# Kernel optimization log

Measured on AMD Instinct MI355X. Metric: run time of the kernel, lower is better.

## Reference

```python
import jax, jax.numpy as jnp
import numpy as np
from jax.scipy.special import erf

B, S, D, H, F = 2, 2048, 1024, 16, 4096
EPS = 1e-5


def setup_inputs() -> dict:
    key = jax.random.key(0)
    ks = jax.random.split(key, 7)
    s = 0.02  # init scale so attention logits stay in a sane range
    return {
        "x": jax.random.normal(ks[0], (B, S, D), jnp.float32),
        "wq": jax.random.normal(ks[1], (D, D), jnp.float32) * s,
        "wk": jax.random.normal(ks[2], (D, D), jnp.float32) * s,
        "wv": jax.random.normal(ks[3], (D, D), jnp.float32) * s,
        "wo": jax.random.normal(ks[4], (D, D), jnp.float32) * s,
        "w1": jax.random.normal(ks[5], (F, D), jnp.float32) * s,
        "w2": jax.random.normal(ks[6], (D, F), jnp.float32) * s,
        "g1": jnp.ones((D,), jnp.float32),
        "g2": jnp.ones((D,), jnp.float32),
    }


def _rmsnorm(x, g):
    return x / jnp.sqrt(jnp.mean(x * x, axis=-1, keepdims=True) + EPS) * g


def _gelu_exact(x):
    # 0.5 * x * (1 + erf(x / sqrt(2)))
    return 0.5 * x * (1.0 + erf(x * (1.0 / np.sqrt(2.0).astype(np.float32))))


def reference(x, wq, wk, wv, wo, w1, w2, g1, g2):
    b, s, d = x.shape
    dk = d // H
    # --- attention sublayer (pre-RMSNorm) ---
    h = _rmsnorm(x, g1)
    # Linear(bias=False): y = h @ W.T; split heads -> [b, H, s, dk]
    q = (h @ wq.T).reshape(b, s, H, dk).transpose(0, 2, 1, 3)
    k = (h @ wk.T).reshape(b, s, H, dk).transpose(0, 2, 1, 3)
    v = (h @ wv.T).reshape(b, s, H, dk).transpose(0, 2, 1, 3)
    scores = jnp.einsum('bhqd,bhkd->bhqk', q, k) / jnp.sqrt(jnp.float32(dk))
    causal = jnp.triu(jnp.ones((s, s), bool), 1)  # True above diagonal -> masked
    scores = jnp.where(causal, -jnp.inf, scores)
    attn = jax.nn.softmax(scores, axis=-1)
    o = jnp.einsum('bhqk,bhkd->bhqd', attn, v)
    o = o.transpose(0, 2, 1, 3).reshape(b, s, d) @ wo.T
    x = x + o
    # --- FFN sublayer (pre-RMSNorm, exact-erf GELU) ---
    h2 = _rmsnorm(x, g2)
    f = _gelu_exact(h2 @ w1.T) @ w2.T
    return x + f
```

## Files before the change

### kernel.cpp

```cpp
#include <hip/hip_runtime.h>
#include <hip/hip_bf16.h>
#include <math.h>

#define B_   2
#define S_   2048
#define D_   1024
#define H_   16
#define DK_  64
#define F_   4096
#define NTOK (B_ * S_)

typedef __bf16 bf16x8 __attribute__((ext_vector_type(8)));
typedef float  f32x4  __attribute__((ext_vector_type(4)));

__device__ __forceinline__ unsigned short bf16r(float f) {
  unsigned u = __builtin_bit_cast(unsigned, f);
  u += 0x7fffu + ((u >> 16) & 1u);
  return (unsigned short)(u >> 16);
}

__device__ __forceinline__ void gload_lds16(const void* g, void* l) {
  __builtin_amdgcn_global_load_lds(
      (__attribute__((address_space(1))) void*)g,
      (__attribute__((address_space(3))) void*)l, 16, 0, 0);
}

__device__ __forceinline__ unsigned lds_off(void* p) {
  return (unsigned)(size_t)(__attribute__((address_space(3))) void*)p;
}
__device__ __forceinline__ bf16x8 ds_read16(unsigned a) {
  bf16x8 r;
  asm volatile("ds_read_b128 %0, %1" : "=v"(r) : "v"(a));
  return r;
}
__device__ __forceinline__ void ds_write32(unsigned a, unsigned v) {
  asm volatile("ds_write_b32 %0, %1" : : "v"(a), "v"(v));
}
__device__ __forceinline__ float fexp2(float x) {
  float r;
  asm volatile("v_exp_f32 %0, %1\n\ts_nop 0" : "=v"(r) : "v"(x));
  return r;
}
__device__ __forceinline__ unsigned cvt_pk_bf16(float lo, float hi) {
  unsigned r;
  asm volatile("v_cvt_pk_bf16_f32 %0, %1, %2" : "=v"(r) : "v"(lo), "v"(hi));
  return r;
}

__device__ __forceinline__ float gelu_fast(float x) {
  float y = 0.7978845608f * x * (1.0f + 0.044715f * x * x);
  float e = fexp2(2.885390082f * y);
  float t = 1.0f - 2.0f / (e + 1.0f);
  return 0.5f * x * (1.0f + t);
}

#define QSCL 0.18033688f

struct CvtArgs {
  const float* src[6];
  unsigned short* dst[6];
  int start[7];
};
__global__ __launch_bounds__(256) void cvt_all_kernel(CvtArgs a) {
  int i = blockIdx.x * blockDim.x + threadIdx.x;
  if (i >= a.start[6]) return;
  int k = 0;
#pragma unroll
  for (int j = 1; j < 6; ++j)
    if (i >= a.start[j]) k = j;
  int off = i - a.start[k];
  float4 v = reinterpret_cast<const float4*>(a.src[k])[off];
  ushort4 o;
  o.x = bf16r(v.x); o.y = bf16r(v.y); o.z = bf16r(v.z); o.w = bf16r(v.w);
  reinterpret_cast<ushort4*>(a.dst[k])[off] = o;
}

__global__ __launch_bounds__(256) void rmsnorm_kernel(
    const float* __restrict__ x, const float* __restrict__ g,
    unsigned short* __restrict__ out) {
  int row = blockIdx.x;
  int t = threadIdx.x, lane = t & 63, w = t >> 6;
  float4 v = reinterpret_cast<const float4*>(x + (size_t)row * D_)[t];
  float ss = v.x * v.x + v.y * v.y + v.z * v.z + v.w * v.w;
#pragma unroll
  for (int d = 1; d < 64; d <<= 1) ss += __shfl_xor(ss, d);
  __shared__ float red[4];
  if (lane == 0) red[w] = ss;
  __syncthreads();
  float tot = red[0] + red[1] + red[2] + red[3];
  float rstd = rsqrtf(tot * (1.0f / D_) + 1e-5f);
  float4 gv = reinterpret_cast<const float4*>(g)[t];
  ushort4 o;
  o.x = bf16r(v.x * rstd * gv.x);
  o.y = bf16r(v.y * rstd * gv.y);
  o.z = bf16r(v.z * rstd * gv.z);
  o.w = bf16r(v.w * rstd * gv.w);
  reinterpret_cast<ushort4*>(out + (size_t)row * D_)[t] = o;
}

template <int EPI>
__device__ __forceinline__ void gemm256_body(
    const unsigned short* __restrict__ A, const unsigned short* __restrict__ Bw,
    int M, int N, int K,
    unsigned short* __restrict__ outB, unsigned short* __restrict__ outB2,
    unsigned short* __restrict__ outB3) {
  constexpr int BUFU = 12288;
  __shared__ __attribute__((aligned(16))) unsigned short lds[3 * BUFU];
  const int t = threadIdx.x, lane = t & 63, w = t >> 6;
  const int wm = w >> 1, wn = w & 1;
  const int lg = lane >> 4, ln = lane & 15;

  const int gx = gridDim.x;
  int bid = blockIdx.y * gx + blockIdx.x;
  int xcd = bid & 7, c = bid >> 3;
  int RX = gx >> 2, RY = gridDim.y >> 1;
  int bx = (xcd & 3) * RX + (c % RX);
  int by = (xcd >> 2) * RY + (c / RX);
  const int m0 = by * 256, n0 = bx * 128;

  const int nt = K >> 5;

  auto stage = [&](int tile) {
    int buf = tile % 3;
    const int k0 = tile << 5;
    unsigned short* la = &lds[buf * BUFU];
    unsigned short* lb = la + 8192;
#pragma unroll
    for (int i = 0; i < 2; ++i) {
      int g = i * 512 + t;
      int Ln = g >> 3, p = g & 7, u = p ^ (Ln & 7);
      int row = 2 * Ln + (u >> 2), cg = u & 3;
      gload_lds16(A + (size_t)(m0 + row) * K + k0 + cg * 8, &la[g * 8]);
    }
    {
      int Ln = t >> 3, p = t & 7, u = p ^ (Ln & 7);
      int row = 2 * Ln + (u >> 2), cg = u & 3;
      gload_lds16(Bw + (size_t)(n0 + row) * K + k0 + cg * 8, &lb[t * 8]);
    }
  };

  stage(0);
  stage(1);

  const unsigned base0 = lds_off(lds);
  unsigned offA[4], offB[4];
#pragma unroll
  for (int m = 0; m < 4; ++m) {
    int r = wm * 64 + m * 16 + ln;
    int Ln = r >> 1, p = ((r & 1) * 4 + lg) ^ (Ln & 7);
    offA[m] = (unsigned)((Ln * 64 + p * 8) * 2);
  }
#pragma unroll
  for (int n = 0; n < 4; ++n) {
    int r = wn * 64 + n * 16 + ln;
    int Ln = r >> 1, p = ((r & 1) * 4 + lg) ^ (Ln & 7);
    offB[n] = (unsigned)(16384 + (Ln * 64 + p * 8) * 2);
  }

  f32x4 acc[4][4] = {};

  for (int tile = 0; tile < nt; ++tile) {
    if (tile + 1 < nt) { asm volatile("s_waitcnt vmcnt(3)"); }
    else               { asm volatile("s_waitcnt vmcnt(0)"); }
    __builtin_amdgcn_sched_barrier(0);
    __builtin_amdgcn_s_barrier();
    const unsigned bb = base0 + (unsigned)((tile % 3) * (BUFU * 2));
    bf16x8 af[4], bf0, bf1;
#pragma unroll
    for (int m = 0; m < 4; ++m) af[m] = ds_read16(bb + offA[m]);
    bf0 = ds_read16(bb + offB[0]);
    bf1 = ds_read16(bb + offB[1]);
    if (tile + 2 < nt) stage(tile + 2);
    asm volatile("s_waitcnt lgkmcnt(0)");
    __builtin_amdgcn_sched_barrier(0);
    __builtin_amdgcn_s_setprio(1);
#pragma unroll
    for (int m = 0; m < 4; ++m) {
      acc[m][0] = __builtin_amdgcn_mfma_f32_16x16x32_bf16(af[m], bf0, acc[m][0], 0, 0, 0);
      acc[m][1] = __builtin_amdgcn_mfma_f32_16x16x32_bf16(af[m], bf1, acc[m][1], 0, 0, 0);
    }
    __builtin_amdgcn_s_setprio(0);
    bf0 = ds_read16(bb + offB[2]);
    bf1 = ds_read16(bb + offB[3]);
    asm volatile("s_waitcnt lgkmcnt(0)");
    __builtin_amdgcn_sched_barrier(0);
    __builtin_amdgcn_s_setprio(1);
#pragma unroll
    for (int m = 0; m < 4; ++m) {
      acc[m][2] = __builtin_amdgcn_mfma_f32_16x16x32_bf16(af[m], bf0, acc[m][2], 0, 0, 0);
      acc[m][3] = __builtin_amdgcn_mfma_f32_16x16x32_bf16(af[m], bf1, acc[m][3], 0, 0, 0);
    }
    __builtin_amdgcn_s_setprio(0);
  }

  const int rbase = m0 + wm * 64 + lg * 4;
  const int cbase = n0 + wn * 64 + ln;
#pragma unroll
  for (int m = 0; m < 4; ++m) {
#pragma unroll
    for (int n = 0; n < 4; ++n) {
      int col = cbase + n * 16;
#pragma unroll
      for (int j = 0; j < 4; ++j) {
        int row = rbase + m * 16 + j;
        float v = acc[m][n][j];
        if (EPI == 1) {
          outB[(size_t)row * N + col] = bf16r(gelu_fast(v));
        } else {
          if (col < D_) {
            outB[(size_t)row * D_ + col] = bf16r(v * QSCL);
          } else if (col < 2 * D_) {
            outB2[(size_t)row * D_ + (col - D_)] = bf16r(v);
          } else {
            int bb2 = row >> 11, s = row & (S_ - 1);
            outB3[((size_t)(bb2 * D_) + (col - 2 * D_)) * S_ + s] = bf16r(v);
          }
        }
      }
    }
  }
}

__global__ __launch_bounds__(512, 4) void qkv_gemm(
    const unsigned short* __restrict__ A, const unsigned short* __restrict__ Bw,
    int M, int N, int K, unsigned short* o1, unsigned short* o2, unsigned short* o3) {
  gemm256_body<4>(A, Bw, M, N, K, o1, o2, o3);
}
__global__ __launch_bounds__(512, 4) void ffn1_gemm(
    const unsigned short* __restrict__ A, const unsigned short* __restrict__ Bw,
    int M, int N, int K, unsigned short* o1) {
  gemm256_body<1>(A, Bw, M, N, K, o1, nullptr, nullptr);
}

__device__ __forceinline__ void gemm128_body(
    const unsigned short* __restrict__ A, const unsigned short* __restrict__ Bw,
    int M, int N, int K,
    const float* __restrict__ resid, float* __restrict__ outF) {
  constexpr int BUFU = 256 * 32;
  __shared__ __attribute__((aligned(16))) unsigned short lds[4 * BUFU];
  const int t = threadIdx.x, lane = t & 63, w = t >> 6;
  const int wm = w >> 2, wn = w & 3;
  const int lg = lane >> 4, ln = lane & 15;

  const int gx = gridDim.x;
  int bid = blockIdx.y * gx + blockIdx.x;
  int RX = gx >> 2, RY = gridDim.y >> 1;
  int xcd = bid & 7, c = bid >> 3;
  int bx = (xcd & 3) * RX + (c % RX);
  int by = (xcd >> 2) * RY + (c / RX);
  const int m0 = by * 128, n0 = bx * 128;

  const int nt = K >> 5;

  auto stage = [&](int tile) {
    const int buf = tile & 3;
    const int k0 = tile << 5;
    unsigned short* la = &lds[buf * BUFU];
    unsigned short* lb = la + 4096;
    int Ln = t >> 3, p = t & 7, u = p ^ (Ln & 7);
    int row = 2 * Ln + (u >> 2), cg = u & 3;
    gload_lds16(A + (size_t)(m0 + row) * K + k0 + cg * 8, &la[t * 8]);
    gload_lds16(Bw + (size_t)(n0 + row) * K + k0 + cg * 8, &lb[t * 8]);
  };

  stage(0);
  if (nt > 1) stage(1);
  if (nt > 2) stage(2);

  const unsigned base0 = lds_off(lds);
  unsigned offA[4], offB[2];
#pragma unroll
  for (int m = 0; m < 4; ++m) {
    int r = wm * 64 + m * 16 + ln;
    int Ln = r >> 1, p = ((r & 1) * 4 + lg) ^ (Ln & 7);
    offA[m] = (unsigned)((Ln * 64 + p * 8) * 2);
  }
#pragma unroll
  for (int n = 0; n < 2; ++n) {
    int r = wn * 32 + n * 16 + ln;
    int Ln = r >> 1, p = ((r & 1) * 4 + lg) ^ (Ln & 7);
    offB[n] = (unsigned)(8192 + (Ln * 64 + p * 8) * 2);
  }

  f32x4 acc[4][2] = {};

  for (int tile = 0; tile < nt; ++tile) {
    const int rem = nt - 1 - tile;
    if (rem >= 2)      { asm volatile("s_waitcnt vmcnt(4)"); }
    else if (rem == 1) { asm volatile("s_waitcnt vmcnt(2)"); }
    else               { asm volatile("s_waitcnt vmcnt(0)"); }
    __builtin_amdgcn_sched_barrier(0);
    __builtin_amdgcn_s_barrier();
    const unsigned bb = base0 + (unsigned)((tile & 3) * (BUFU * 2));
    bf16x8 af[4], bf[2];
#pragma unroll
    for (int m = 0; m < 4; ++m) af[m] = ds_read16(bb + offA[m]);
#pragma unroll
    for (int n = 0; n < 2; ++n) bf[n] = ds_read16(bb + offB[n]);
    if (tile + 3 < nt) stage(tile + 3);
    asm volatile("s_waitcnt lgkmcnt(0)");
    __builtin_amdgcn_sched_barrier(0);
    __builtin_amdgcn_s_setprio(1);
#pragma unroll
    for (int m = 0; m < 4; ++m)
#pragma unroll
      for (int n = 0; n < 2; ++n)
        acc[m][n] = __builtin_amdgcn_mfma_f32_16x16x32_bf16(af[m], bf[n], acc[m][n], 0, 0, 0);
    __builtin_amdgcn_s_setprio(0);
  }

  const int rbase = m0 + wm * 64 + lg * 4;
  const int cbase = n0 + wn * 32 + ln;
#pragma unroll
  for (int m = 0; m < 4; ++m) {
#pragma unroll
    for (int n = 0; n < 2; ++n) {
      int col = cbase + n * 16;
#pragma unroll
      for (int j = 0; j < 4; ++j) {
        int row = rbase + m * 16 + j;
        outF[(size_t)row * N + col] = acc[m][n][j] + resid[(size_t)row * N + col];
      }
    }
  }
}

__global__ __launch_bounds__(512, 4) void wo_gemm(
    const unsigned short* __restrict__ A, const unsigned short* __restrict__ Bw,
    int M, int N, int K, const float* __restrict__ resid, float* __restrict__ outF) {
  gemm128_body(A, Bw, M, N, K, resid, outF);
}
__global__ __launch_bounds__(512, 4) void ffn2_gemm(
    const unsigned short* __restrict__ A, const unsigned short* __restrict__ Bw,
    int M, int N, int K, const float* __restrict__ resid, float* __restrict__ outF) {
  gemm128_body(A, Bw, M, N, K, resid, outF);
}

__global__ __launch_bounds__(256, 4) void attn_kernel(
    const unsigned short* __restrict__ qg, const unsigned short* __restrict__ kg,
    const unsigned short* __restrict__ vt, unsigned short* __restrict__ og) {
  __shared__ __attribute__((aligned(16))) unsigned short Kl[2][4096];
  __shared__ __attribute__((aligned(16))) unsigned short Vl[2][4096];
  __shared__ __attribute__((aligned(16))) unsigned short Pl[4][1024];
  const int t = threadIdx.x, lane = t & 63, w = t >> 6;
  const int lg = lane >> 4, ln = lane & 15;

  int bid = blockIdx.x;
  int nl = (bid & 7) * 128 + (bid >> 3);
  int bh = nl >> 5, qxr = nl & 31;
  int b = bh >> 4, h = bh & 15;
  int q0 = (31 - qxr) * 64;
  int qw = q0 + w * 16;

  bf16x8 aq[2];
  {
    const unsigned short* qp =
        qg + (size_t)(b * S_ + qw + ln) * D_ + h * DK_ + lg * 8;
    aq[0] = *reinterpret_cast<const bf16x8*>(qp);
    aq[1] = *reinterpret_cast<const bf16x8*>(qp + 32);
  }
  asm volatile("" : : "v"(aq[0]), "v"(aq[1]));

  float mr = -1e30f, lr = 0.f;
  f32x4 oacc[4] = {};
  const int nt = (q0 >> 6) + 1;

  auto stage = [&](int kt) {
    const int buf = kt & 1;
    const int kv0 = kt * 64;
#pragma unroll
    for (int i = 0; i < 2; ++i) {
      int g = i * 256 + t;
      int row = g >> 3, cg = g & 7, sg = cg ^ (row & 7);
      gload_lds16(kg + (size_t)(b * S_ + kv0 + row) * D_ + h * DK_ + sg * 8, &Kl[buf][g * 8]);
      gload_lds16(vt + (size_t)(b * D_ + h * DK_ + row) * S_ + kv0 + sg * 8, &Vl[buf][g * 8]);
    }
  };
  stage(0);

  const unsigned kbase = lds_off(&Kl[0][0]);
  const unsigned vbase = lds_off(&Vl[0][0]);
  const unsigned pbase = lds_off(&Pl[w][0]);

  auto ctile = [&](int kt, bool dm) {
    const unsigned kb = kbase + (unsigned)((kt & 1) * 8192);
    const unsigned vb = vbase + (unsigned)((kt & 1) * 8192);
    f32x4 sc[4] = {};
    bf16x8 kf[4];
#pragma unroll
    for (int n = 0; n < 4; ++n) {
      int r = n * 16 + ln;
      int cg0 = lg ^ (r & 7);
      kf[n] = ds_read16(kb + (unsigned)((r * 64 + cg0 * 8) * 2));
    }
    if (!dm) stage(kt + 1);
    asm volatile("s_waitcnt lgkmcnt(0)");
    __builtin_amdgcn_sched_barrier(0);
#pragma unroll
    for (int n = 0; n < 4; ++n)
      sc[n] = __builtin_amdgcn_mfma_f32_16x16x32_bf16(kf[n], aq[0], sc[n], 0, 0, 0);
#pragma unroll
    for (int n = 0; n < 4; ++n) {
      int r = n * 16 + ln;
      int cg1 = (4 + lg) ^ (r & 7);
      kf[n] = ds_read16(kb + (unsigned)((r * 64 + cg1 * 8) * 2));
    }
    asm volatile("s_waitcnt lgkmcnt(0)");
    __builtin_amdgcn_sched_barrier(0);
#pragma unroll
    for (int n = 0; n < 4; ++n)
      sc[n] = __builtin_amdgcn_mfma_f32_16x16x32_bf16(kf[n], aq[1], sc[n], 0, 0, 0);
    if (dm) {
      const int kv0 = kt * 64;
      const int qi = qw + ln;
#pragma unroll
      for (int n = 0; n < 4; ++n)
#pragma unroll
        for (int j = 0; j < 4; ++j)
          if ((kv0 + n * 16 + lg * 4 + j) > qi) sc[n][j] = -1e30f;
    }
    float t0 = fmaxf(sc[0][0], sc[0][1]), t1 = fmaxf(sc[0][2], sc[0][3]);
    float t2 = fmaxf(sc[1][0], sc[1][1]), t3 = fmaxf(sc[1][2], sc[1][3]);
    float t4 = fmaxf(sc[2][0], sc[2][1]), t5 = fmaxf(sc[2][2], sc[2][3]);
    float t6 = fmaxf(sc[3][0], sc[3][1]), t7 = fmaxf(sc[3][2], sc[3][3]);
    t0 = fmaxf(t0, t1); t2 = fmaxf(t2, t3); t4 = fmaxf(t4, t5); t6 = fmaxf(t6, t7);
    float mx = fmaxf(fmaxf(t0, t2), fmaxf(t4, t6));
    mx = fmaxf(mx, __shfl_xor(mx, 16));
    mx = fmaxf(mx, __shfl_xor(mx, 32));
    float mn = fmaxf(mr, mx);
    float ps = 0.f;
#pragma unroll
    for (int n = 0; n < 4; ++n)
#pragma unroll
      for (int j = 0; j < 4; ++j) {
        float p = fexp2(sc[n][j] - mn);
        sc[n][j] = p;
        ps += p;
      }
    if (__all(mx <= mr)) {
      lr += ps;
    } else {
      float sf = fexp2(mr - mn);
      mr = mn;
      lr = lr * sf + ps;
#pragma unroll
      for (int j = 0; j < 4; ++j) {
        float sfj = __shfl(sf, lg * 4 + j);
#pragma unroll
        for (int f = 0; f < 4; ++f) oacc[f][j] *= sfj;
      }
    }
#pragma unroll
    for (int n = 0; n < 4; ++n) {
      int kvc = n * 16 + lg * 4;
      int cg = (kvc >> 3) ^ (ln & 7);
      unsigned pa_addr = pbase + (unsigned)((ln * 64 + cg * 8 + (kvc & 7)) * 2);
      ds_write32(pa_addr, cvt_pk_bf16(sc[n][0], sc[n][1]));
      ds_write32(pa_addr + 4, cvt_pk_bf16(sc[n][2], sc[n][3]));
    }
    asm volatile("s_waitcnt lgkmcnt(0)");
    __builtin_amdgcn_sched_barrier(0);
#pragma unroll
    for (int c = 0; c < 2; ++c) {
      unsigned cgp = (unsigned)((c * 4 + lg) ^ (ln & 7));
      bf16x8 pa = ds_read16(pbase + (unsigned)(ln * 128) + cgp * 16);
      bf16x8 vf[4];
#pragma unroll
      for (int f = 0; f < 4; ++f) {
        int dv = f * 16 + ln;
        int cgv = (c * 4 + lg) ^ (dv & 7);
        vf[f] = ds_read16(vb + (unsigned)((dv * 64 + cgv * 8) * 2));
      }
      asm volatile("s_waitcnt lgkmcnt(0)");
      __builtin_amdgcn_sched_barrier(0);
#pragma unroll
      for (int f = 0; f < 4; ++f)
        oacc[f] = __builtin_amdgcn_mfma_f32_16x16x32_bf16(pa, vf[f], oacc[f], 0, 0, 0);
    }
  };

  for (int kt = 0; kt < nt - 1; ++kt) {
    asm volatile("s_waitcnt vmcnt(0)");
    __builtin_amdgcn_sched_barrier(0);
    __builtin_amdgcn_s_barrier();
    ctile(kt, false);
  }
  asm volatile("s_waitcnt vmcnt(0)");
  __builtin_amdgcn_sched_barrier(0);
  __builtin_amdgcn_s_barrier();
  ctile(nt - 1, true);

  lr += __shfl_xor(lr, 16);
  lr += __shfl_xor(lr, 32);
#pragma unroll
  for (int j = 0; j < 4; ++j) {
    float lj = __shfl(lr, lg * 4 + j);
    float inv = 1.0f / lj;
    int row = b * S_ + qw + lg * 4 + j;
#pragma unroll
    for (int f = 0; f < 4; ++f)
      og[(size_t)row * D_ + h * DK_ + f * 16 + ln] = bf16r(oacc[f][j] * inv);
  }
}

extern "C" void kernel_launch(void* const* d_in, const int* in_sizes, int n_in,
                              void* d_out, int out_size, void* d_ws, size_t ws_size,
                              hipStream_t stream) {
  const float* x  = (const float*)d_in[0];
  const float* wq = (const float*)d_in[1];
  const float* wk = (const float*)d_in[2];
  const float* wv = (const float*)d_in[3];
  const float* wo = (const float*)d_in[4];
  const float* w1 = (const float*)d_in[5];
  const float* w2 = (const float*)d_in[6];
  const float* g1 = (const float*)d_in[7];
  const float* g2 = (const float*)d_in[8];
  float* out = (float*)d_out;

  char* ws = (char*)d_ws;
  const size_t MB = 1024 * 1024;
  unsigned short* wqkv_b = (unsigned short*)(ws + 0 * MB);
  unsigned short* wo_b   = (unsigned short*)(ws + 6 * MB);
  unsigned short* w1_b   = (unsigned short*)(ws + 8 * MB);
  unsigned short* w2_b   = (unsigned short*)(ws + 16 * MB);
  unsigned short* h_b    = (unsigned short*)(ws + 24 * MB);
  unsigned short* q_b    = (unsigned short*)(ws + 32 * MB);
  unsigned short* k_b    = (unsigned short*)(ws + 40 * MB);
  unsigned short* vt_b   = (unsigned short*)(ws + 48 * MB);
  unsigned short* o_b    = (unsigned short*)(ws + 56 * MB);
  float*          x1     = (float*)(ws + 64 * MB);
  unsigned short* mid    = (unsigned short*)(ws + 80 * MB);

  CvtArgs ca;
  ca.src[0] = wq; ca.dst[0] = wqkv_b;
  ca.src[1] = wk; ca.dst[1] = wqkv_b + (size_t)D_ * D_;
  ca.src[2] = wv; ca.dst[2] = wqkv_b + (size_t)2 * D_ * D_;
  ca.src[3] = wo; ca.dst[3] = wo_b;
  ca.src[4] = w1; ca.dst[4] = w1_b;
  ca.src[5] = w2; ca.dst[5] = w2_b;
  int q4 = D_ * D_ / 4, f4 = F_ * D_ / 4;
  ca.start[0] = 0;
  ca.start[1] = q4;
  ca.start[2] = 2 * q4;
  ca.start[3] = 3 * q4;
  ca.start[4] = 4 * q4;
  ca.start[5] = 4 * q4 + f4;
  ca.start[6] = 4 * q4 + 2 * f4;
  cvt_all_kernel<<<(ca.start[6] + 255) / 256, 256, 0, stream>>>(ca);

  rmsnorm_kernel<<<NTOK, 256, 0, stream>>>(x, g1, h_b);

  qkv_gemm<<<dim3(3 * D_ / 128, NTOK / 256), dim3(512), 0, stream>>>(
      h_b, wqkv_b, NTOK, 3 * D_, D_, q_b, k_b, vt_b);

  attn_kernel<<<dim3(1024), dim3(256), 0, stream>>>(q_b, k_b, vt_b, o_b);

  wo_gemm<<<dim3(D_ / 128, NTOK / 128), dim3(512), 0, stream>>>(
      o_b, wo_b, NTOK, D_, D_, x, x1);

  rmsnorm_kernel<<<NTOK, 256, 0, stream>>>(x1, g2, h_b);

  ffn1_gemm<<<dim3(F_ / 128, NTOK / 256), dim3(512), 0, stream>>>(
      h_b, w1_b, NTOK, F_, D_, mid);

  ffn2_gemm<<<dim3(D_ / 128, NTOK / 128), dim3(512), 0, stream>>>(
      mid, w2_b, NTOK, D_, F_, x1, out);
}
```

Baseline: 248.8 us.

## Enlarge GEMM tiles to 256x256 and pair causal query tiles with 128-wide KV tiles

The shared QKV/FFN1 GEMM body now computes 256x256 output tiles instead of 256x128. Each warp handles 128 rows, and the A and B halves of the next stage are staged separately, interleaved with the two MFMA halves. The attention kernel now uses 128-key K/V tiles and has each block process two query tiles (31-pi and pi), so causal work is balanced across blocks while the grid is halved. This targets operand reuse and load imbalance, at the cost of a larger LDS footprint, lower occupancy (launch bounds drop to 2), and fewer blocks in the QKV GEMM (192) to spread over the CUs.

```diff
diff --git a/kernel.cpp b/kernel.cpp
--- a/kernel.cpp
+++ b/kernel.cpp
@@ -104,10 +104,10 @@
     int M, int N, int K,
     unsigned short* __restrict__ outB, unsigned short* __restrict__ outB2,
     unsigned short* __restrict__ outB3) {
-  constexpr int BUFU = 12288;
+  constexpr int BUFU = 16384;
   __shared__ __attribute__((aligned(16))) unsigned short lds[3 * BUFU];
   const int t = threadIdx.x, lane = t & 63, w = t >> 6;
-  const int wm = w >> 1, wn = w & 1;
+  const int wm = w >> 2, wn = w & 3;
   const int lg = lane >> 4, ln = lane & 15;
 
   const int gx = gridDim.x;
@@ -116,15 +116,13 @@
   int RX = gx >> 2, RY = gridDim.y >> 1;
   int bx = (xcd & 3) * RX + (c % RX);
   int by = (xcd >> 2) * RY + (c / RX);
-  const int m0 = by * 256, n0 = bx * 128;
+  const int m0 = by * 256, n0 = bx * 256;
 
   const int nt = K >> 5;
 
-  auto stage = [&](int tile) {
-    int buf = tile % 3;
+  auto stageA = [&](int tile) {
+    unsigned short* la = &lds[(tile % 3) * BUFU];
     const int k0 = tile << 5;
-    unsigned short* la = &lds[buf * BUFU];
-    unsigned short* lb = la + 8192;
 #pragma unroll
     for (int i = 0; i < 2; ++i) {
       int g = i * 512 + t;
@@ -132,21 +130,27 @@
       int row = 2 * Ln + (u >> 2), cg = u & 3;
       gload_lds16(A + (size_t)(m0 + row) * K + k0 + cg * 8, &la[g * 8]);
     }
-    {
-      int Ln = t >> 3, p = t & 7, u = p ^ (Ln & 7);
+  };
+  auto stageB = [&](int tile) {
+    unsigned short* lb = &lds[(tile % 3) * BUFU + 8192];
+    const int k0 = tile << 5;
+#pragma unroll
+    for (int i = 0; i < 2; ++i) {
+      int g = i * 512 + t;
+      int Ln = g >> 3, p = g & 7, u = p ^ (Ln & 7);
       int row = 2 * Ln + (u >> 2), cg = u & 3;
-      gload_lds16(Bw + (size_t)(n0 + row) * K + k0 + cg * 8, &lb[t * 8]);
+      gload_lds16(Bw + (size_t)(n0 + row) * K + k0 + cg * 8, &lb[g * 8]);
     }
   };
 
-  stage(0);
-  stage(1);
+  stageA(0); stageB(0);
+  stageA(1); stageB(1);
 
   const unsigned base0 = lds_off(lds);
-  unsigned offA[4], offB[4];
-#pragma unroll
-  for (int m = 0; m < 4; ++m) {
-    int r = wm * 64 + m * 16 + ln;
+  unsigned offA[8], offB[4];
+#pragma unroll
+  for (int m = 0; m < 8; ++m) {
+    int r = wm * 128 + m * 16 + ln;
     int Ln = r >> 1, p = ((r & 1) * 4 + lg) ^ (Ln & 7);
     offA[m] = (unsigned)((Ln * 64 + p * 8) * 2);
   }
@@ -157,46 +161,48 @@
     offB[n] = (unsigned)(16384 + (Ln * 64 + p * 8) * 2);
   }
 
-  f32x4 acc[4][4] = {};
+  f32x4 acc[8][4] = {};
 
   for (int tile = 0; tile < nt; ++tile) {
-    if (tile + 1 < nt) { asm volatile("s_waitcnt vmcnt(3)"); }
+    if (tile + 1 < nt) { asm volatile("s_waitcnt vmcnt(4)"); }
     else               { asm volatile("s_waitcnt vmcnt(0)"); }
     __builtin_amdgcn_sched_barrier(0);
     __builtin_amdgcn_s_barrier();
     const unsigned bb = base0 + (unsigned)((tile % 3) * (BUFU * 2));
-    bf16x8 af[4], bf0, bf1;
+    bf16x8 af[4], bf[4], af2[4];
 #pragma unroll
     for (int m = 0; m < 4; ++m) af[m] = ds_read16(bb + offA[m]);
-    bf0 = ds_read16(bb + offB[0]);
-    bf1 = ds_read16(bb + offB[1]);
-    if (tile + 2 < nt) stage(tile + 2);
+#pragma unroll
+    for (int n = 0; n < 4; ++n) bf[n] = ds_read16(bb + offB[n]);
+    if (tile + 2 < nt) stageA(tile + 2);
     asm volatile("s_waitcnt lgkmcnt(0)");
     __builtin_amdgcn_sched_barrier(0);
     __builtin_amdgcn_s_setprio(1);
 #pragma unroll
-    for (int m = 0; m < 4; ++m) {
-      acc[m][0] = __builtin_amdgcn_mfma_f32_16x16x32_bf16(af[m], bf0, acc[m][0], 0, 0, 0);
-      acc[m][1] = __builtin_amdgcn_mfma_f32_16x16x32_bf16(af[m], bf1, acc[m][1], 0, 0, 0);
-    }
+    for (int m = 0; m < 4; ++m)
+#pragma unroll
+      for (int n = 0; n < 4; ++n)
+        acc[m][n] = __builtin_amdgcn_mfma_f32_16x16x32_bf16(af[m], bf[n], acc[m][n], 0, 0, 0);
     __builtin_amdgcn_s_setprio(0);
-    bf0 = ds_read16(bb + offB[2]);
-    bf1 = ds_read16(bb + offB[3]);
+    __builtin_amdgcn_s_barrier();
+#pragma unroll
+    for (int m = 0; m < 4; ++m) af2[m] = ds_read16(bb + offA[4 + m]);
+    if (tile + 2 < nt) stageB(tile + 2);
     asm volatile("s_waitcnt lgkmcnt(0)");
     __builtin_amdgcn_sched_barrier(0);
     __builtin_amdgcn_s_setprio(1);
 #pragma unroll
-    for (int m = 0; m < 4; ++m) {
-      acc[m][2] = __builtin_amdgcn_mfma_f32_16x16x32_bf16(af[m], bf0, acc[m][2], 0, 0, 0);
-      acc[m][3] = __builtin_amdgcn_mfma_f32_16x16x32_bf16(af[m], bf1, acc[m][3], 0, 0, 0);
-    }
+    for (int m = 0; m < 4; ++m)
+#pragma unroll
+      for (int n = 0; n < 4; ++n)
+        acc[4 + m][n] = __builtin_amdgcn_mfma_f32_16x16x32_bf16(af2[m], bf[n], acc[4 + m][n], 0, 0, 0);
     __builtin_amdgcn_s_setprio(0);
   }
 
-  const int rbase = m0 + wm * 64 + lg * 4;
+  const int rbase = m0 + wm * 128 + lg * 4;
   const int cbase = n0 + wn * 64 + ln;
 #pragma unroll
-  for (int m = 0; m < 4; ++m) {
+  for (int m = 0; m < 8; ++m) {
 #pragma unroll
     for (int n = 0; n < 4; ++n) {
       int col = cbase + n * 16;
@@ -221,12 +227,12 @@
   }
 }
 
-__global__ __launch_bounds__(512, 4) void qkv_gemm(
+__global__ __launch_bounds__(512, 2) void qkv_gemm(
     const unsigned short* __restrict__ A, const unsigned short* __restrict__ Bw,
     int M, int N, int K, unsigned short* o1, unsigned short* o2, unsigned short* o3) {
   gemm256_body<4>(A, Bw, M, N, K, o1, o2, o3);
 }
-__global__ __launch_bounds__(512, 4) void ffn1_gemm(
+__global__ __launch_bounds__(512, 2) void ffn1_gemm(
     const unsigned short* __restrict__ A, const unsigned short* __restrict__ Bw,
     int M, int N, int K, unsigned short* o1) {
   gemm256_body<1>(A, Bw, M, N, K, o1, nullptr, nullptr);
@@ -336,171 +342,186 @@
   gemm128_body(A, Bw, M, N, K, resid, outF);
 }
 
-__global__ __launch_bounds__(256, 4) void attn_kernel(
+__global__ __launch_bounds__(256, 2) void attn_kernel(
     const unsigned short* __restrict__ qg, const unsigned short* __restrict__ kg,
     const unsigned short* __restrict__ vt, unsigned short* __restrict__ og) {
-  __shared__ __attribute__((aligned(16))) unsigned short Kl[2][4096];
-  __shared__ __attribute__((aligned(16))) unsigned short Vl[2][4096];
-  __shared__ __attribute__((aligned(16))) unsigned short Pl[4][1024];
+  __shared__ __attribute__((aligned(16))) unsigned short Kl[2][8192];
+  __shared__ __attribute__((aligned(16))) unsigned short Vl[2][8192];
+  __shared__ __attribute__((aligned(16))) unsigned short Pl[4][2048];
   const int t = threadIdx.x, lane = t & 63, w = t >> 6;
   const int lg = lane >> 4, ln = lane & 15;
 
   int bid = blockIdx.x;
-  int nl = (bid & 7) * 128 + (bid >> 3);
-  int bh = nl >> 5, qxr = nl & 31;
+  int nl = (bid & 7) * 64 + (bid >> 3);
+  int bh = nl >> 4, pi = nl & 15;
   int b = bh >> 4, h = bh & 15;
-  int q0 = (31 - qxr) * 64;
-  int qw = q0 + w * 16;
-
-  bf16x8 aq[2];
-  {
-    const unsigned short* qp =
-        qg + (size_t)(b * S_ + qw + ln) * D_ + h * DK_ + lg * 8;
-    aq[0] = *reinterpret_cast<const bf16x8*>(qp);
-    aq[1] = *reinterpret_cast<const bf16x8*>(qp + 32);
-  }
-  asm volatile("" : : "v"(aq[0]), "v"(aq[1]));
-
-  float mr = -1e30f, lr = 0.f;
-  f32x4 oacc[4] = {};
-  const int nt = (q0 >> 6) + 1;
-
-  auto stage = [&](int kt) {
-    const int buf = kt & 1;
-    const int kv0 = kt * 64;
-#pragma unroll
-    for (int i = 0; i < 2; ++i) {
-      int g = i * 256 + t;
-      int row = g >> 3, cg = g & 7, sg = cg ^ (row & 7);
-      gload_lds16(kg + (size_t)(b * S_ + kv0 + row) * D_ + h * DK_ + sg * 8, &Kl[buf][g * 8]);
-      gload_lds16(vt + (size_t)(b * D_ + h * DK_ + row) * S_ + kv0 + sg * 8, &Vl[buf][g * 8]);
-    }
-  };
-  stage(0);
 
   const unsigned kbase = lds_off(&Kl[0][0]);
   const unsigned vbase = lds_off(&Vl[0][0]);
   const unsigned pbase = lds_off(&Pl[w][0]);
 
-  auto ctile = [&](int kt, bool dm) {
-    const unsigned kb = kbase + (unsigned)((kt & 1) * 8192);
-    const unsigned vb = vbase + (unsigned)((kt & 1) * 8192);
-    f32x4 sc[4] = {};
-    bf16x8 kf[4];
-#pragma unroll
-    for (int n = 0; n < 4; ++n) {
-      int r = n * 16 + ln;
-      int cg0 = lg ^ (r & 7);
-      kf[n] = ds_read16(kb + (unsigned)((r * 64 + cg0 * 8) * 2));
-    }
-    if (!dm) stage(kt + 1);
-    asm volatile("s_waitcnt lgkmcnt(0)");
-    __builtin_amdgcn_sched_barrier(0);
-#pragma unroll
-    for (int n = 0; n < 4; ++n)
-      sc[n] = __builtin_amdgcn_mfma_f32_16x16x32_bf16(kf[n], aq[0], sc[n], 0, 0, 0);
-#pragma unroll
-    for (int n = 0; n < 4; ++n) {
-      int r = n * 16 + ln;
-      int cg1 = (4 + lg) ^ (r & 7);
-      kf[n] = ds_read16(kb + (unsigned)((r * 64 + cg1 * 8) * 2));
-    }
-    asm volatile("s_waitcnt lgkmcnt(0)");
-    __builtin_amdgcn_sched_barrier(0);
-#pragma unroll
-    for (int n = 0; n < 4; ++n)
-      sc[n] = __builtin_amdgcn_mfma_f32_16x16x32_bf16(kf[n], aq[1], sc[n], 0, 0, 0);
-    if (dm) {
-      const int kv0 = kt * 64;
-      const int qi = qw + ln;
-#pragma unroll
-      for (int n = 0; n < 4; ++n)
-#pragma unroll
-        for (int j = 0; j < 4; ++j)
-          if ((kv0 + n * 16 + lg * 4 + j) > qi) sc[n][j] = -1e30f;
-    }
-    float t0 = fmaxf(sc[0][0], sc[0][1]), t1 = fmaxf(sc[0][2], sc[0][3]);
-    float t2 = fmaxf(sc[1][0], sc[1][1]), t3 = fmaxf(sc[1][2], sc[1][3]);
-    float t4 = fmaxf(sc[2][0], sc[2][1]), t5 = fmaxf(sc[2][2], sc[2][3]);
-    float t6 = fmaxf(sc[3][0], sc[3][1]), t7 = fmaxf(sc[3][2], sc[3][3]);
-    t0 = fmaxf(t0, t1); t2 = fmaxf(t2, t3); t4 = fmaxf(t4, t5); t6 = fmaxf(t6, t7);
-    float mx = fmaxf(fmaxf(t0, t2), fmaxf(t4, t6));
-    mx = fmaxf(mx, __shfl_xor(mx, 16));
-    mx = fmaxf(mx, __shfl_xor(mx, 32));
-    float mn = fmaxf(mr, mx);
-    float ps = 0.f;
-#pragma unroll
-    for (int n = 0; n < 4; ++n)
-#pragma unroll
-      for (int j = 0; j < 4; ++j) {
-        float p = fexp2(sc[n][j] - mn);
-        sc[n][j] = p;
-        ps += p;
-      }
-    if (__all(mx <= mr)) {
-      lr += ps;
-    } else {
-      float sf = fexp2(mr - mn);
-      mr = mn;
-      lr = lr * sf + ps;
-#pragma unroll
-      for (int j = 0; j < 4; ++j) {
-        float sfj = __shfl(sf, lg * 4 + j);
-#pragma unroll
-        for (int f = 0; f < 4; ++f) oacc[f][j] *= sfj;
-      }
-    }
-#pragma unroll
-    for (int n = 0; n < 4; ++n) {
-      int kvc = n * 16 + lg * 4;
-      int cg = (kvc >> 3) ^ (ln & 7);
-      unsigned pa_addr = pbase + (unsigned)((ln * 64 + cg * 8 + (kvc & 7)) * 2);
-      ds_write32(pa_addr, cvt_pk_bf16(sc[n][0], sc[n][1]));
-      ds_write32(pa_addr + 4, cvt_pk_bf16(sc[n][2], sc[n][3]));
-    }
-    asm volatile("s_waitcnt lgkmcnt(0)");
-    __builtin_amdgcn_sched_barrier(0);
-#pragma unroll
-    for (int c = 0; c < 2; ++c) {
-      unsigned cgp = (unsigned)((c * 4 + lg) ^ (ln & 7));
-      bf16x8 pa = ds_read16(pbase + (unsigned)(ln * 128) + cgp * 16);
-      bf16x8 vf[4];
-#pragma unroll
-      for (int f = 0; f < 4; ++f) {
-        int dv = f * 16 + ln;
-        int cgv = (c * 4 + lg) ^ (dv & 7);
-        vf[f] = ds_read16(vb + (unsigned)((dv * 64 + cgv * 8) * 2));
-      }
+  auto runq = [&](int qtile, bool first) {
+    const int q0 = qtile * 64;
+    const int qw = q0 + w * 16;
+    const int nt = (q0 >> 7) + 1;
+
+    bf16x8 aq[2];
+    {
+      const unsigned short* qp =
+          qg + (size_t)(b * S_ + qw + ln) * D_ + h * DK_ + lg * 8;
+      aq[0] = *reinterpret_cast<const bf16x8*>(qp);
+      aq[1] = *reinterpret_cast<const bf16x8*>(qp + 32);
+    }
+    asm volatile("" : : "v"(aq[0]), "v"(aq[1]));
+
+    float mr = -1e30f, lr = 0.f;
+    f32x4 oacc[4] = {};
+
+    auto stage = [&](int kt) {
+      const int buf = kt & 1;
+      const int kv0 = kt * 128;
+#pragma unroll
+      for (int i = 0; i < 4; ++i) {
+        int g = i * 256 + t;
+        int row = g >> 3, cg = g & 7, sg = cg ^ (row & 7);
+        gload_lds16(kg + (size_t)(b * S_ + kv0 + row) * D_ + h * DK_ + sg * 8,
+                    &Kl[buf][g * 8]);
+      }
+#pragma unroll
+      for (int i = 0; i < 4; ++i) {
+        int g = i * 256 + t;
+        int row = g >> 4, cg = g & 15, sg = cg ^ (row & 15);
+        gload_lds16(vt + (size_t)(b * D_ + h * DK_ + row) * S_ + kv0 + sg * 8,
+                    &Vl[buf][g * 8]);
+      }
+    };
+
+    if (!first) __builtin_amdgcn_s_barrier();
+    stage(0);
+
+    auto ctile = [&](int kt, bool dm) {
+      const unsigned kb = kbase + (unsigned)((kt & 1) * 16384);
+      const unsigned vb = vbase + (unsigned)((kt & 1) * 16384);
+      f32x4 sc[8] = {};
+      bf16x8 kf[8];
+#pragma unroll
+      for (int n = 0; n < 8; ++n) {
+        int r = n * 16 + ln;
+        int cg0 = lg ^ (r & 7);
+        kf[n] = ds_read16(kb + (unsigned)((r * 128 + cg0 * 16)));
+      }
+      if (!dm) stage(kt + 1);
       asm volatile("s_waitcnt lgkmcnt(0)");
       __builtin_amdgcn_sched_barrier(0);
 #pragma unroll
-      for (int f = 0; f < 4; ++f)
-        oacc[f] = __builtin_amdgcn_mfma_f32_16x16x32_bf16(pa, vf[f], oacc[f], 0, 0, 0);
-    }
-  };
-
-  for (int kt = 0; kt < nt - 1; ++kt) {
+      for (int n = 0; n < 8; ++n)
+        sc[n] = __builtin_amdgcn_mfma_f32_16x16x32_bf16(kf[n], aq[0], sc[n], 0, 0, 0);
+#pragma unroll
+      for (int n = 0; n < 8; ++n) {
+        int r = n * 16 + ln;
+        int cg1 = (4 + lg) ^ (r & 7);
+        kf[n] = ds_read16(kb + (unsigned)((r * 128 + cg1 * 16)));
+      }
+      asm volatile("s_waitcnt lgkmcnt(0)");
+      __builtin_amdgcn_sched_barrier(0);
+#pragma unroll
+      for (int n = 0; n < 8; ++n)
+        sc[n] = __builtin_amdgcn_mfma_f32_16x16x32_bf16(kf[n], aq[1], sc[n], 0, 0, 0);
+      if (dm) {
+        const int kv0 = kt * 128;
+        const int qi = qw + ln;
+#pragma unroll
+        for (int n = 0; n < 8; ++n)
+#pragma unroll
+          for (int j = 0; j < 4; ++j)
+            if ((kv0 + n * 16 + lg * 4 + j) > qi) sc[n][j] = -1e30f;
+      }
+      float mx = -1e30f;
+#pragma unroll
+      for (int n = 0; n < 8; ++n) {
+        float a = fmaxf(fmaxf(sc[n][0], sc[n][1]), fmaxf(sc[n][2], sc[n][3]));
+        mx = fmaxf(mx, a);
+      }
+      mx = fmaxf(mx, __shfl_xor(mx, 16));
+      mx = fmaxf(mx, __shfl_xor(mx, 32));
+      float mn = fmaxf(mr, mx);
+      float ps = 0.f;
+#pragma unroll
+      for (int n = 0; n < 8; ++n)
+#pragma unroll
+        for (int j = 0; j < 4; ++j) {
+          float p = fexp2(sc[n][j] - mn);
+          sc[n][j] = p;
+          ps += p;
+        }
+      if (__all(mx <= mr)) {
+        lr += ps;
+      } else {
+        float sf = fexp2(mr - mn);
+        mr = mn;
+        lr = lr * sf + ps;
+#pragma unroll
+        for (int j = 0; j < 4; ++j) {
+          float sfj = __shfl(sf, lg * 4 + j);
+#pragma unroll
+          for (int f = 0; f < 4; ++f) oacc[f][j] *= sfj;
+        }
+      }
+#pragma unroll
+      for (int n = 0; n < 8; ++n) {
+        int kvc = n * 16 + lg * 4;
+        int gsw = ((kvc >> 3) ^ ln) & 15;
+        unsigned pa_addr = pbase + (unsigned)(ln * 256 + gsw * 16 + (kvc & 7) * 2);
+        ds_write32(pa_addr, cvt_pk_bf16(sc[n][0], sc[n][1]));
+        ds_write32(pa_addr + 4, cvt_pk_bf16(sc[n][2], sc[n][3]));
+      }
+      asm volatile("s_waitcnt lgkmcnt(0)");
+      __builtin_amdgcn_sched_barrier(0);
+#pragma unroll
+      for (int c = 0; c < 4; ++c) {
+        unsigned cgp = (unsigned)(((c * 4 + lg) ^ ln) & 15);
+        bf16x8 pa = ds_read16(pbase + (unsigned)(ln * 256) + cgp * 16);
+        bf16x8 vf[4];
+#pragma unroll
+        for (int f = 0; f < 4; ++f) {
+          int dv = f * 16 + ln;
+          int cgv = ((c * 4 + lg) ^ (dv & 15)) & 15;
+          vf[f] = ds_read16(vb + (unsigned)(dv * 256 + cgv * 16));
+        }
+        asm volatile("s_waitcnt lgkmcnt(0)");
+        __builtin_amdgcn_sched_barrier(0);
+#pragma unroll
+        for (int f = 0; f < 4; ++f)
+          oacc[f] = __builtin_amdgcn_mfma_f32_16x16x32_bf16(pa, vf[f], oacc[f], 0, 0, 0);
+      }
+    };
+
+    for (int kt = 0; kt < nt - 1; ++kt) {
+      asm volatile("s_waitcnt vmcnt(0)");
+      __builtin_amdgcn_sched_barrier(0);
+      __builtin_amdgcn_s_barrier();
+      ctile(kt, false);
+    }
     asm volatile("s_waitcnt vmcnt(0)");
     __builtin_amdgcn_sched_barrier(0);
     __builtin_amdgcn_s_barrier();
-    ctile(kt, false);
-  }
-  asm volatile("s_waitcnt vmcnt(0)");
-  __builtin_amdgcn_sched_barrier(0);
-  __builtin_amdgcn_s_barrier();
-  ctile(nt - 1, true);
-
-  lr += __shfl_xor(lr, 16);
-  lr += __shfl_xor(lr, 32);
-#pragma unroll
-  for (int j = 0; j < 4; ++j) {
-    float lj = __shfl(lr, lg * 4 + j);
-    float inv = 1.0f / lj;
-    int row = b * S_ + qw + lg * 4 + j;
-#pragma unroll
-    for (int f = 0; f < 4; ++f)
-      og[(size_t)row * D_ + h * DK_ + f * 16 + ln] = bf16r(oacc[f][j] * inv);
-  }
+    ctile(nt - 1, true);
+
+    lr += __shfl_xor(lr, 16);
+    lr += __shfl_xor(lr, 32);
+#pragma unroll
+    for (int j = 0; j < 4; ++j) {
+      float lj = __shfl(lr, lg * 4 + j);
+      float inv = 1.0f / lj;
+      int row = b * S_ + qw + lg * 4 + j;
+#pragma unroll
+      for (int f = 0; f < 4; ++f)
+        og[(size_t)row * D_ + h * DK_ + f * 16 + ln] = bf16r(oacc[f][j] * inv);
+    }
+  };
+
+  runq(31 - pi, true);
+  runq(pi, false);
 }
 
 extern "C" void kernel_launch(void* const* d_in, const int* in_sizes, int n_in,
@@ -550,17 +571,17 @@
 
   rmsnorm_kernel<<<NTOK, 256, 0, stream>>>(x, g1, h_b);
 
-  qkv_gemm<<<dim3(3 * D_ / 128, NTOK / 256), dim3(512), 0, stream>>>(
+  qkv_gemm<<<dim3(3 * D_ / 256, NTOK / 256), dim3(512), 0, stream>>>(
       h_b, wqkv_b, NTOK, 3 * D_, D_, q_b, k_b, vt_b);
 
-  attn_kernel<<<dim3(1024), dim3(256), 0, stream>>>(q_b, k_b, vt_b, o_b);
+  attn_kernel<<<dim3(512), dim3(256), 0, stream>>>(q_b, k_b, vt_b, o_b);
 
   wo_gemm<<<dim3(D_ / 128, NTOK / 128), dim3(512), 0, stream>>>(
       o_b, wo_b, NTOK, D_, D_, x, x1);
 
   rmsnorm_kernel<<<NTOK, 256, 0, stream>>>(x1, g2, h_b);
 
-  ffn1_gemm<<<dim3(F_ / 128, NTOK / 256), dim3(512), 0, stream>>>(
+  ffn1_gemm<<<dim3(F_ / 256, NTOK / 256), dim3(512), 0, stream>>>(
       h_b, w1_b, NTOK, F_, D_, mid);
 
   ffn2_gemm<<<dim3(D_ / 128, NTOK / 128), dim3(512), 0, stream>>>(
```

After: 252.2 us. Within noise of the previous version (+1.4%).
